# Performance work log

Measured on AMD Instinct MI355X. Metric: run time of the kernel, lower is better.

The kernel has to match this reference:

```python
import jax, jax.numpy as jnp
import numpy as np

IN_FEATURES = 1024
OUT_FEATURES = 1024
GRID_SIZE = 5
SPLINE_ORDER = 3
N_BASIS = GRID_SIZE + SPLINE_ORDER  # 8, matches spline_weight last dim
N_GRID = GRID_SIZE + 2 * SPLINE_ORDER + 1  # 12 knots -> Cox-de-Boor yields N_BASIS bases


def b_spline(x, grid):
    # x: [B, I] -> bases: [B, I, N_BASIS]
    x = x[..., None]
    bases = ((x >= grid[:-1]) & (x < grid[1:])).astype(x.dtype)
    for k in range(1, SPLINE_ORDER + 1):
        left = (x - grid[: -k - 1]) / (grid[k:-1] - grid[: -k - 1] + 1e-8)
        right = (grid[k + 1:] - x) / (grid[k + 1:] - grid[1:-k] + 1e-8)
        bases = left * bases[..., :-1] + right * bases[..., 1:]
    return bases


def setup_inputs() -> dict:
    key = jax.random.key(0)
    k1, k2, k3 = jax.random.split(key, 3)
    x = jax.random.uniform(k1, (4096, IN_FEATURES), dtype=jnp.float32) * 2.0 - 1.0
    # kaiming_uniform_(a=sqrt(5)) on [out,in]: bound = 1/sqrt(in)
    bound = 1.0 / np.sqrt(IN_FEATURES)
    base_weight = jax.random.uniform(k2, (OUT_FEATURES, IN_FEATURES), dtype=jnp.float32,
                                     minval=-bound, maxval=bound)
    spline_weight = 0.1 * jax.random.normal(k3, (OUT_FEATURES, IN_FEATURES, N_BASIS), dtype=jnp.float32)
    grid = jnp.linspace(-1.0, 1.0, N_GRID, dtype=jnp.float32)
    return {"x": x, "base_weight": base_weight, "spline_weight": spline_weight, "grid": grid}


def reference(x, base_weight, spline_weight, grid):
    base_output = jax.nn.silu(x) @ base_weight.T  # [B, O]
    spline_basis = b_spline(x, grid)              # [B, I, Q]
    spline_output = jnp.einsum('biq,oiq->bo', spline_basis, spline_weight)
    return base_output + spline_output
```

## Files before the change

kernel.cpp:

```cpp
#include <hip/hip_runtime.h>
#include <hip/hip_bf16.h>

#define IN_F 1024
#define OUT_F 1024
#define QP 9
#define KDIM (IN_F * QP)
#define SPLITK 2
#define KSLICE (KDIM / SPLITK)
#define BK 64

typedef __attribute__((ext_vector_type(8)))  short short8;
typedef __attribute__((ext_vector_type(16))) float floatx16;
typedef __attribute__((ext_vector_type(8)))  unsigned short ushort8v;

__device__ __forceinline__ unsigned short f2bf(float f) {
    union { float f; unsigned u; } v; v.f = f;
    return (unsigned short)((v.u + 0x7FFF + ((v.u >> 16) & 1)) >> 16);
}
__device__ __forceinline__ float bf2f(unsigned short h) {
    union { unsigned u; float f; } v; v.u = ((unsigned)h) << 16;
    return v.f;
}

__global__ __launch_bounds__(256) void pack_kernel(const float* __restrict__ x,
                                                   const float* __restrict__ bw,
                                                   const float* __restrict__ sw,
                                                   __hip_bfloat16* __restrict__ A,
                                                   __hip_bfloat16* __restrict__ W, int Bm) {
    const int nb_a = (Bm * IN_F / 8) / 256;
    if ((int)blockIdx.x < nb_a) {
        int t  = blockIdx.x * 256 + threadIdx.x;
        int b  = t >> 7;
        int i0 = (t & 127) * 8;
        const float4* xr = (const float4*)(x + (size_t)b * IN_F + i0);
        float4 x0 = xr[0], x1 = xr[1];
        float xv[8] = {x0.x, x0.y, x0.z, x0.w, x1.x, x1.y, x1.z, x1.w};
        ushort8v ov[9];
#pragma unroll
        for (int e = 0; e < 8; ++e) {
            float v  = xv[e];
            float u  = (v + 1.0f) * 5.5f;
            float fj = floorf(u);
            int   j  = (int)fj;
            float tt = u - fj;
            float t2 = tt * tt, t3 = t2 * tt;
            float omt = 1.0f - tt;
            float w0 = omt * omt * omt * (1.0f / 6.0f);
            float w1 = (3.0f * t3 - 6.0f * t2 + 4.0f) * (1.0f / 6.0f);
            float w2 = (-3.0f * t3 + 3.0f * t2 + 3.0f * tt + 1.0f) * (1.0f/6.0f);
            float w3 = t3 * (1.0f / 6.0f);
            ov[0][e] = f2bf(v * __builtin_amdgcn_rcpf(1.0f + __expf(-v)));
#pragma unroll
            for (int q = 0; q < 8; ++q) {
                int d = j - q;
                float bv = (d == 3) ? w0 : (d == 2) ? w1 : (d == 1) ? w2 : (d == 0) ? w3 : 0.0f;
                ov[1 + q][e] = f2bf(bv);
            }
        }
        unsigned short* dst = (unsigned short*)A + (size_t)b * KDIM + i0;
#pragma unroll
        for (int s = 0; s < QP; ++s)
            *(ushort8v*)(dst + (size_t)s * IN_F) = ov[s];
    } else {
        int t = ((int)blockIdx.x - nb_a) * 256 + threadIdx.x;
        unsigned short* dst = (unsigned short*)W + (size_t)(t >> 10) * KDIM + (t & 1023);
        dst[0] = f2bf(bw[t]);
        const float4* s4 = (const float4*)(sw + (size_t)t * 8);
        float4 lo = s4[0], hi = s4[1];
        dst[1 * IN_F] = f2bf(lo.x); dst[2 * IN_F] = f2bf(lo.y);
        dst[3 * IN_F] = f2bf(lo.z); dst[4 * IN_F] = f2bf(lo.w);
        dst[5 * IN_F] = f2bf(hi.x); dst[6 * IN_F] = f2bf(hi.y);
        dst[7 * IN_F] = f2bf(hi.z); dst[8 * IN_F] = f2bf(hi.w);
    }
}

__global__ __launch_bounds__(256, 2) void gemm_splitk(const __hip_bfloat16* __restrict__ A,
                                                      const __hip_bfloat16* __restrict__ W,
                                                      unsigned short* __restrict__ P, int Bm) {
    __shared__ short sA[128 * BK];
    __shared__ short sB[128 * BK];
    const int tid   = threadIdx.x;
    const int lane  = tid & 63;
    const int wave  = tid >> 6;
    const int row32 = lane & 31;
    const int half  = lane >> 5;
    const int wm = wave >> 1, wn = wave & 1;
    const int m0 = blockIdx.y * 128;
    const int n0 = blockIdx.x * 128;
    const int kb = blockIdx.z * KSLICE;

    const short* Ag = (const short*)A + (size_t)m0 * KDIM + kb;
    const short* Wg = (const short*)W + (size_t)n0 * KDIM + kb;

    floatx16 acc[2][2] = {};

    int rs[4], ko[4], ld[4];
#pragma unroll
    for (int p = 0; p < 4; ++p) {
        int c = p * 256 + tid;
        rs[p] = c >> 3;
        ko[p] = (((c & 7) ^ ((rs[p] >> 1) & 7)) * 8);
        ld[p] = c * 8;
    }

    const int rA0 = wm * 64 + row32, rA1 = rA0 + 32;
    const int rB0 = wn * 64 + row32, rB1 = rB0 + 32;
    const int swA0 = (rA0 >> 1) & 7, swA1 = (rA1 >> 1) & 7;
    const int swB0 = (rB0 >> 1) & 7, swB1 = (rB1 >> 1) & 7;

    for (int k0 = 0; k0 < KSLICE; k0 += BK) {
#pragma unroll
        for (int p = 0; p < 4; ++p)
            __builtin_amdgcn_global_load_lds(
                (const __attribute__((address_space(1))) void*)(Ag + (size_t)rs[p] * KDIM + k0 + ko[p]),
                (__attribute__((address_space(3))) void*)(sA + ld[p]), 16, 0, 0);
#pragma unroll
        for (int p = 0; p < 4; ++p)
            __builtin_amdgcn_global_load_lds(
                (const __attribute__((address_space(1))) void*)(Wg + (size_t)rs[p] * KDIM + k0 + ko[p]),
                (__attribute__((address_space(3))) void*)(sB + ld[p]), 16, 0, 0);
        __syncthreads();

#pragma unroll
        for (int ks = 0; ks < 4; ++ks) {
            int c = ks * 2 + half;
            short8 aF[2], bF[2];
            aF[0] = *(const short8*)&sA[rA0 * BK + ((c ^ swA0) * 8)];
            aF[1] = *(const short8*)&sA[rA1 * BK + ((c ^ swA1) * 8)];
            bF[0] = *(const short8*)&sB[rB0 * BK + ((c ^ swB0) * 8)];
            bF[1] = *(const short8*)&sB[rB1 * BK + ((c ^ swB1) * 8)];
#pragma unroll
            for (int mi = 0; mi < 2; ++mi)
#pragma unroll
                for (int ni = 0; ni < 2; ++ni)
                    acc[mi][ni] = __builtin_amdgcn_mfma_f32_32x32x16_bf16(
                        aF[mi], bF[ni], acc[mi][ni], 0, 0, 0);
        }
        __syncthreads();
    }

    unsigned short* Pz = P + (size_t)blockIdx.z * Bm * OUT_F;
#pragma unroll
    for (int mi = 0; mi < 2; ++mi)
#pragma unroll
        for (int ni = 0; ni < 2; ++ni)
#pragma unroll
            for (int r = 0; r < 16; ++r) {
                int row = (r & 3) + 8 * (r >> 2) + 4 * half;
                int gm  = m0 + wm * 64 + mi * 32 + row;
                Pz[(size_t)gm * OUT_F + n0 + wn * 64 + ni * 32 + row32] = f2bf(acc[mi][ni][r]);
            }
}

__global__ __launch_bounds__(256) void reduce_kernel(const unsigned short* __restrict__ P,
                                                     float* __restrict__ C, int n) {
    int t  = blockIdx.x * 256 + threadIdx.x;
    int i0 = t * 8;
    ushort8v a = *(const ushort8v*)(P + i0);
    ushort8v b = *(const ushort8v*)(P + (size_t)n + i0);
    float4 o0, o1;
    o0.x = bf2f(a[0]) + bf2f(b[0]); o0.y = bf2f(a[1]) + bf2f(b[1]);
    o0.z = bf2f(a[2]) + bf2f(b[2]); o0.w = bf2f(a[3]) + bf2f(b[3]);
    o1.x = bf2f(a[4]) + bf2f(b[4]); o1.y = bf2f(a[5]) + bf2f(b[5]);
    o1.z = bf2f(a[6]) + bf2f(b[6]); o1.w = bf2f(a[7]) + bf2f(b[7]);
    *(float4*)(C + i0)     = o0;
    *(float4*)(C + i0 + 4) = o1;
}

__global__ __launch_bounds__(256) void fallback_kernel(const float* __restrict__ x,
                                                       const float* __restrict__ bw,
                                                       const float* __restrict__ sw,
                                                       const float* __restrict__ grid,
                                                       float* __restrict__ out, int Bm) {
    __shared__ float sv[256][QP + 1];
    int b = blockIdx.y;
    int o = blockIdx.x * 256 + threadIdx.x;
    float acc = 0.f;
    for (int ic = 0; ic < IN_F; ic += 256) {
        int i = ic + threadIdx.x;
        float v = x[(size_t)b * IN_F + i];
        float g[12];
        for (int j = 0; j < 12; ++j) g[j] = grid[j];
        float bb[11];
        for (int j = 0; j < 11; ++j) bb[j] = (v >= g[j] && v < g[j + 1]) ? 1.f : 0.f;
        for (int k = 1; k <= 3; ++k)
            for (int j = 0; j < 11 - k; ++j)
                bb[j] = (v - g[j]) / (g[j + k] - g[j] + 1e-8f) * bb[j]
                      + (g[j + k + 1] - v) / (g[j + k + 1] - g[j + 1] + 1e-8f) * bb[j + 1];
        __syncthreads();
        sv[threadIdx.x][0] = v / (1.f + __expf(-v));
        for (int q = 0; q < 8; ++q) sv[threadIdx.x][1 + q] = bb[q];
        __syncthreads();
        for (int ii = 0; ii < 256; ++ii) {
            int i2 = ic + ii;
            acc += sv[ii][0] * bw[(size_t)o * IN_F + i2];
            const float* swp = sw + ((size_t)o * IN_F + i2) * 8;
            for (int q = 0; q < 8; ++q) acc += sv[ii][1 + q] * swp[q];
        }
    }
    out[(size_t)b * OUT_F + o] = acc;
}

extern "C" void kernel_launch(void* const* d_in, const int* in_sizes, int n_in,
                              void* d_out, int out_size, void* d_ws, size_t ws_size,
                              hipStream_t stream) {
    const float* x    = (const float*)d_in[0];
    const float* bw   = (const float*)d_in[1];
    const float* sw   = (const float*)d_in[2];
    const float* grid = (const float*)d_in[3];
    float* out = (float*)d_out;

    const int Bm = in_sizes[0] / IN_F;
    const size_t a_bytes = (size_t)Bm * KDIM * sizeof(__hip_bfloat16);
    const size_t w_bytes = (size_t)OUT_F * KDIM * sizeof(__hip_bfloat16);
    const size_t p_bytes = (size_t)SPLITK * Bm * OUT_F * sizeof(unsigned short);

    if (ws_size >= a_bytes + w_bytes + p_bytes && (Bm % 128) == 0) {
        __hip_bfloat16* Apk = (__hip_bfloat16*)d_ws;
        __hip_bfloat16* Wpk = (__hip_bfloat16*)((char*)d_ws + a_bytes);
        unsigned short* P = (unsigned short*)((char*)d_ws + a_bytes + w_bytes);
        const int nb_a = (Bm * IN_F / 8) / 256;
        const int nb_w = (OUT_F * IN_F) / 256;
        pack_kernel<<<nb_a + nb_w, 256, 0, stream>>>(x, bw, sw, Apk, Wpk, Bm);
        gemm_splitk<<<dim3(OUT_F / 128, Bm / 128, SPLITK), 256, 0, stream>>>(Apk, Wpk, P, Bm);
        reduce_kernel<<<Bm * OUT_F / 2048, 256, 0, stream>>>(P, out, Bm * OUT_F);
    } else {
        fallback_kernel<<<dim3(OUT_F / 256, Bm), 256, 0, stream>>>(x, bw, sw, grid, out, Bm);
    }
}
```

Baseline: 215.0 us.

## Restructure split-K GEMM into 256x256 tiles with triple-buffered async LDS pipeline

```diff
diff --git a/kernel.cpp b/kernel.cpp
--- a/kernel.cpp
+++ b/kernel.cpp
@@ -5,9 +5,9 @@
 #define OUT_F 1024
 #define QP 9
 #define KDIM (IN_F * QP)
-#define SPLITK 2
-#define KSLICE (KDIM / SPLITK)
-#define BK 64
+#define BM 256
+#define BN 256
+#define BK 32
 
 typedef __attribute__((ext_vector_type(8)))  short short8;
 typedef __attribute__((ext_vector_type(16))) float floatx16;
@@ -74,95 +74,136 @@
     }
 }
 
-__global__ __launch_bounds__(256, 2) void gemm_splitk(const __hip_bfloat16* __restrict__ A,
+#define GLD(src, dst) __builtin_amdgcn_global_load_lds( \
+        (const __attribute__((address_space(1))) void*)(src), \
+        (__attribute__((address_space(3))) void*)(dst), 16, 0, 0)
+
+__global__ __launch_bounds__(512, 2) void gemm_splitk(const __hip_bfloat16* __restrict__ A,
                                                       const __hip_bfloat16* __restrict__ W,
-                                                      unsigned short* __restrict__ P, int Bm) {
-    __shared__ short sA[128 * BK];
-    __shared__ short sB[128 * BK];
-    const int tid   = threadIdx.x;
-    const int lane  = tid & 63;
-    const int wave  = tid >> 6;
-    const int row32 = lane & 31;
-    const int half  = lane >> 5;
-    const int wm = wave >> 1, wn = wave & 1;
-    const int m0 = blockIdx.y * 128;
-    const int n0 = blockIdx.x * 128;
-    const int kb = blockIdx.z * KSLICE;
+                                                      unsigned short* __restrict__ P,
+                                                      int Bm, int splitk, int kslice) {
+    __shared__ short sA[3][BM * BK];
+    __shared__ short sB[3][BN * BK];
+    const int tid  = threadIdx.x;
+    const int lane = tid & 63;
+    const int wave = tid >> 6;
+    const int r32  = lane & 31;
+    const int half = lane >> 5;
+    const int wm   = wave >> 2;
+    const int wn   = wave & 3;
+
+    const int b   = (int)blockIdx.x;
+    const int xcd = b & 7, ii = b >> 3;
+    const int pp  = xcd * (splitk >> 1) + (ii >> 4);
+    const int xt  = pp & 3, zt = pp >> 2, yt = ii & 15;
+    const int m0 = yt * BM, n0 = xt * BN, kb = zt * kslice;
+    const int NT = kslice / BK;
 
     const short* Ag = (const short*)A + (size_t)m0 * KDIM + kb;
     const short* Wg = (const short*)W + (size_t)n0 * KDIM + kb;
 
-    floatx16 acc[2][2] = {};
-
-    int rs[4], ko[4], ld[4];
-#pragma unroll
-    for (int p = 0; p < 4; ++p) {
-        int c = p * 256 + tid;
-        rs[p] = c >> 3;
-        ko[p] = (((c & 7) ^ ((rs[p] >> 1) & 7)) * 8);
-        ld[p] = c * 8;
-    }
-
-    const int rA0 = wm * 64 + row32, rA1 = rA0 + 32;
-    const int rB0 = wn * 64 + row32, rB1 = rB0 + 32;
-    const int swA0 = (rA0 >> 1) & 7, swA1 = (rA1 >> 1) & 7;
-    const int swB0 = (rB0 >> 1) & 7, swB1 = (rB1 >> 1) & 7;
-
-    for (int k0 = 0; k0 < KSLICE; k0 += BK) {
-#pragma unroll
-        for (int p = 0; p < 4; ++p)
-            __builtin_amdgcn_global_load_lds(
-                (const __attribute__((address_space(1))) void*)(Ag + (size_t)rs[p] * KDIM + k0 + ko[p]),
-                (__attribute__((address_space(3))) void*)(sA + ld[p]), 16, 0, 0);
-#pragma unroll
-        for (int p = 0; p < 4; ++p)
-            __builtin_amdgcn_global_load_lds(
-                (const __attribute__((address_space(1))) void*)(Wg + (size_t)rs[p] * KDIM + k0 + ko[p]),
-                (__attribute__((address_space(3))) void*)(sB + ld[p]), 16, 0, 0);
-        __syncthreads();
-
-#pragma unroll
-        for (int ks = 0; ks < 4; ++ks) {
-            int c = ks * 2 + half;
-            short8 aF[2], bF[2];
-            aF[0] = *(const short8*)&sA[rA0 * BK + ((c ^ swA0) * 8)];
-            aF[1] = *(const short8*)&sA[rA1 * BK + ((c ^ swA1) * 8)];
-            bF[0] = *(const short8*)&sB[rB0 * BK + ((c ^ swB0) * 8)];
-            bF[1] = *(const short8*)&sB[rB1 * BK + ((c ^ swB1) * 8)];
-#pragma unroll
-            for (int mi = 0; mi < 2; ++mi)
+    const int c0 = tid, c1 = 512 + tid;
+    const int g0 = (c0 & 3) ^ ((c0 >> 3) & 3);
+    const int g1 = (c1 & 3) ^ ((c1 >> 3) & 3);
+    const short* pA0 = Ag + (size_t)(c0 >> 2) * KDIM + g0 * 8;
+    const short* pA1 = Ag + (size_t)(c1 >> 2) * KDIM + g1 * 8;
+    const short* pB0 = Wg + (size_t)(c0 >> 2) * KDIM + g0 * 8;
+    const short* pB1 = Wg + (size_t)(c1 >> 2) * KDIM + g1 * 8;
+    const int l0 = c0 * 8, l1 = c1 * 8;
+
+    int offA[4][2], offB[2][2];
+#pragma unroll
+    for (int mi = 0; mi < 4; ++mi) {
+        int row = wm * 128 + mi * 32 + r32;
+        int sw  = (row >> 1) & 3;
+#pragma unroll
+        for (int kc = 0; kc < 2; ++kc)
+            offA[mi][kc] = row * BK + (((kc * 2 + half) ^ sw) * 8);
+    }
+#pragma unroll
+    for (int ni = 0; ni < 2; ++ni) {
+        int row = wn * 64 + ni * 32 + r32;
+        int sw  = (row >> 1) & 3;
+#pragma unroll
+        for (int kc = 0; kc < 2; ++kc)
+            offB[ni][kc] = row * BK + (((kc * 2 + half) ^ sw) * 8);
+    }
+
+    floatx16 acc[4][2] = {};
+
+#define STAGE(bi, koff) do { \
+        GLD(pA0 + (koff), &sA[bi][l0]); \
+        GLD(pA1 + (koff), &sA[bi][l1]); \
+        GLD(pB0 + (koff), &sB[bi][l0]); \
+        GLD(pB1 + (koff), &sB[bi][l1]); \
+    } while (0)
+
+    STAGE(0, 0);
+    STAGE(1, BK);
+
+    int bi = 0;
+    for (int t = 0; t < NT; ++t) {
+        if (t == NT - 1) asm volatile("s_waitcnt vmcnt(0) lgkmcnt(0)" ::: "memory");
+        else             asm volatile("s_waitcnt vmcnt(4) lgkmcnt(0)" ::: "memory");
+        __builtin_amdgcn_s_barrier();
+
+        const short* sAb = &sA[bi][0];
+        const short* sBb = &sB[bi][0];
+        short8 aF[2][4], bF[2][2];
+#pragma unroll
+        for (int kc = 0; kc < 2; ++kc) {
+#pragma unroll
+            for (int mi = 0; mi < 4; ++mi) aF[kc][mi] = *(const short8*)(sAb + offA[mi][kc]);
+#pragma unroll
+            for (int ni = 0; ni < 2; ++ni) bF[kc][ni] = *(const short8*)(sBb + offB[ni][kc]);
+        }
+
+        if (t + 2 < NT) {
+            int b2 = bi + 2; if (b2 >= 3) b2 -= 3;
+            STAGE(b2, (t + 2) * BK);
+        }
+
+        __builtin_amdgcn_s_setprio(1);
+#pragma unroll
+        for (int kc = 0; kc < 2; ++kc)
+#pragma unroll
+            for (int mi = 0; mi < 4; ++mi)
 #pragma unroll
                 for (int ni = 0; ni < 2; ++ni)
                     acc[mi][ni] = __builtin_amdgcn_mfma_f32_32x32x16_bf16(
-                        aF[mi], bF[ni], acc[mi][ni], 0, 0, 0);
-        }
-        __syncthreads();
-    }
-
-    unsigned short* Pz = P + (size_t)blockIdx.z * Bm * OUT_F;
-#pragma unroll
-    for (int mi = 0; mi < 2; ++mi)
+                        aF[kc][mi], bF[kc][ni], acc[mi][ni], 0, 0, 0);
+        __builtin_amdgcn_s_setprio(0);
+
+        if (++bi == 3) bi = 0;
+    }
+#undef STAGE
+
+    unsigned short* Pz = P + (size_t)zt * Bm * OUT_F;
+#pragma unroll
+    for (int mi = 0; mi < 4; ++mi)
 #pragma unroll
         for (int ni = 0; ni < 2; ++ni)
 #pragma unroll
             for (int r = 0; r < 16; ++r) {
                 int row = (r & 3) + 8 * (r >> 2) + 4 * half;
-                int gm  = m0 + wm * 64 + mi * 32 + row;
-                Pz[(size_t)gm * OUT_F + n0 + wn * 64 + ni * 32 + row32] = f2bf(acc[mi][ni][r]);
+                int gm  = m0 + wm * 128 + mi * 32 + row;
+                Pz[(size_t)gm * OUT_F + n0 + wn * 64 + ni * 32 + r32] = f2bf(acc[mi][ni][r]);
             }
 }
 
 __global__ __launch_bounds__(256) void reduce_kernel(const unsigned short* __restrict__ P,
-                                                     float* __restrict__ C, int n) {
+                                                     float* __restrict__ C, int n, int s) {
     int t  = blockIdx.x * 256 + threadIdx.x;
     int i0 = t * 8;
-    ushort8v a = *(const ushort8v*)(P + i0);
-    ushort8v b = *(const ushort8v*)(P + (size_t)n + i0);
+    float o[8] = {0.f, 0.f, 0.f, 0.f, 0.f, 0.f, 0.f, 0.f};
+    for (int j = 0; j < s; ++j) {
+        ushort8v a = *(const ushort8v*)(P + (size_t)j * n + i0);
+#pragma unroll
+        for (int e = 0; e < 8; ++e) o[e] += bf2f(a[e]);
+    }
     float4 o0, o1;
-    o0.x = bf2f(a[0]) + bf2f(b[0]); o0.y = bf2f(a[1]) + bf2f(b[1]);
-    o0.z = bf2f(a[2]) + bf2f(b[2]); o0.w = bf2f(a[3]) + bf2f(b[3]);
-    o1.x = bf2f(a[4]) + bf2f(b[4]); o1.y = bf2f(a[5]) + bf2f(b[5]);
-    o1.z = bf2f(a[6]) + bf2f(b[6]); o1.w = bf2f(a[7]) + bf2f(b[7]);
+    o0.x = o[0]; o0.y = o[1]; o0.z = o[2]; o0.w = o[3];
+    o1.x = o[4]; o1.y = o[5]; o1.z = o[6]; o1.w = o[7];
     *(float4*)(C + i0)     = o0;
     *(float4*)(C + i0 + 4) = o1;
 }
@@ -213,17 +254,24 @@
     const int Bm = in_sizes[0] / IN_F;
     const size_t a_bytes = (size_t)Bm * KDIM * sizeof(__hip_bfloat16);
     const size_t w_bytes = (size_t)OUT_F * KDIM * sizeof(__hip_bfloat16);
-    const size_t p_bytes = (size_t)SPLITK * Bm * OUT_F * sizeof(unsigned short);
-
-    if (ws_size >= a_bytes + w_bytes + p_bytes && (Bm % 128) == 0) {
+
+    int splitk = 4;
+    size_t p_bytes = (size_t)splitk * Bm * OUT_F * sizeof(unsigned short);
+    if (ws_size < a_bytes + w_bytes + p_bytes) {
+        splitk = 2;
+        p_bytes = (size_t)splitk * Bm * OUT_F * sizeof(unsigned short);
+    }
+
+    if (ws_size >= a_bytes + w_bytes + p_bytes && Bm == 4096) {
         __hip_bfloat16* Apk = (__hip_bfloat16*)d_ws;
         __hip_bfloat16* Wpk = (__hip_bfloat16*)((char*)d_ws + a_bytes);
         unsigned short* P = (unsigned short*)((char*)d_ws + a_bytes + w_bytes);
         const int nb_a = (Bm * IN_F / 8) / 256;
         const int nb_w = (OUT_F * IN_F) / 256;
         pack_kernel<<<nb_a + nb_w, 256, 0, stream>>>(x, bw, sw, Apk, Wpk, Bm);
-        gemm_splitk<<<dim3(OUT_F / 128, Bm / 128, SPLITK), 256, 0, stream>>>(Apk, Wpk, P, Bm);
-        reduce_kernel<<<Bm * OUT_F / 2048, 256, 0, stream>>>(P, out, Bm * OUT_F);
+        gemm_splitk<<<(Bm / BM) * (OUT_F / BN) * splitk, 512, 0, stream>>>(
+            Apk, Wpk, P, Bm, splitk, KDIM / splitk);
+        reduce_kernel<<<Bm * OUT_F / 2048, 256, 0, stream>>>(P, out, Bm * OUT_F, splitk);
     } else {
         fallback_kernel<<<dim3(OUT_F / 256, Bm), 256, 0, stream>>>(x, bw, sw, grid, out, Bm);
     }
```

Result: faster. 200.0 us (-7.0%).
